# Kernel tuning notes

Measured on AMD Instinct MI355X. Metric: run time of the kernel, lower is better.

## Reference

```python
import jax, jax.numpy as jnp
import numpy as np

P = 16         # patch size
D = 192        # embed dim (vit_tiny)
NH = 3         # heads
DEPTH = 12
HID = 768      # mlp hidden = 4*D
NCLS = 1000
PCT = 0.25
EPS = 1e-6


def _ln(x, s, b):
    m = x.mean(-1, keepdims=True)
    v = ((x - m) ** 2).mean(-1, keepdims=True)
    return (x - m) * jax.lax.rsqrt(v + EPS) * s + b


def setup_inputs() -> dict:
    key = jax.random.key(0)
    ks = jax.random.split(key, 24)
    B, IMG = 64, 384
    std = 0.02
    d = {
        "magno_image": jax.random.normal(ks[0], (B, 3, IMG, IMG), jnp.float32),
        "line_drawing": jax.random.uniform(ks[1], (B, 1, IMG, IMG), jnp.float32),
        "conv_w": jax.random.normal(ks[2], (D, 3, P, P), jnp.float32) * std,
        "conv_b": jnp.zeros((D,), jnp.float32),
        "pos_embed": jax.random.normal(ks[3], (1, (IMG // P) ** 2 + 1, D), jnp.float32) * std,
        "cls_token": jax.random.normal(ks[4], (1, 1, D), jnp.float32) * std,
        "ln1_s": jnp.ones((DEPTH, D), jnp.float32),
        "ln1_b": jnp.zeros((DEPTH, D), jnp.float32),
        "qkv_w": jax.random.normal(ks[5], (DEPTH, D, 3 * D), jnp.float32) * std,
        "qkv_b": jnp.zeros((DEPTH, 3 * D), jnp.float32),
        "proj_w": jax.random.normal(ks[6], (DEPTH, D, D), jnp.float32) * std,
        "proj_b": jnp.zeros((DEPTH, D), jnp.float32),
        "ln2_s": jnp.ones((DEPTH, D), jnp.float32),
        "ln2_b": jnp.zeros((DEPTH, D), jnp.float32),
        "fc1_w": jax.random.normal(ks[7], (DEPTH, D, HID), jnp.float32) * std,
        "fc1_b": jnp.zeros((DEPTH, HID), jnp.float32),
        "fc2_w": jax.random.normal(ks[8], (DEPTH, HID, D), jnp.float32) * std,
        "fc2_b": jnp.zeros((DEPTH, D), jnp.float32),
        "normf_s": jnp.ones((D,), jnp.float32),
        "normf_b": jnp.zeros((D,), jnp.float32),
        "head_w": jax.random.normal(ks[9], (D, NCLS), jnp.float32) * std,
        "head_b": jnp.zeros((NCLS,), jnp.float32),
    }
    return d


def _forward(magno_image, line_drawing, conv_w, conv_b, pos_embed, cls_token,
             ln1_s, ln1_b, qkv_w, qkv_b, proj_w, proj_b, ln2_s, ln2_b,
             fc1_w, fc1_b, fc2_w, fc2_b, normf_s, normf_b, head_w, head_b):
    B, _, IMG, _ = magno_image.shape
    g = IMG // P
    N = g * g
    k = int(N * PCT)
    hd = D // NH

    # --- PatchImportanceScorer: avg-pool(patch_size) then flatten ---
    scores = line_drawing.reshape(B, g, P, g, P).mean(axis=(2, 4)).reshape(B, N)

    # --- patch embed (conv stride == kernel == reshaped matmul) ---
    x = magno_image.reshape(B, 3, g, P, g, P).transpose(0, 2, 4, 1, 3, 5)
    patches = x.reshape(B, N, 3 * P * P) @ conv_w.reshape(D, 3 * P * P).T + conv_b

    # --- top_k selection + gather of patches and pos-embed ---
    _, idx = jax.lax.top_k(scores, k)                      # (B, k)
    sel = jnp.take_along_axis(patches, idx[:, :, None], axis=1)
    pos = jnp.take_along_axis(
        jnp.broadcast_to(pos_embed[:, 1:, :], (B, N, D)), idx[:, :, None], axis=1)
    sel = sel + pos

    cls = jnp.broadcast_to(cls_token + pos_embed[:, :1, :], (B, 1, D))
    seq = jnp.concatenate([cls, sel], axis=1)              # (B, 1+k, D)
    S = 1 + k

    def block(h, p):
        l1s, l1b, qw, qb, pw, pb, l2s, l2b, f1w, f1b, f2w, f2b = p
        y = _ln(h, l1s, l1b)
        qkv = (y @ qw + qb).reshape(B, S, 3, NH, hd)
        q, kk, v = qkv[:, :, 0], qkv[:, :, 1], qkv[:, :, 2]  # (B,S,NH,hd)
        att = jnp.einsum('bqhd,bkhd->bhqk', q, kk) / np.sqrt(hd).astype(np.float32)
        att = jax.nn.softmax(att, axis=-1)
        o = jnp.einsum('bhqk,bkhd->bqhd', att, v).reshape(B, S, D)
        h = h + o @ pw + pb
        y = _ln(h, l2s, l2b)
        h = h + jax.nn.gelu(y @ f1w + f1b, approximate=False) @ f2w + f2b
        return h, None

    seq, _ = jax.lax.scan(block, seq, (ln1_s, ln1_b, qkv_w, qkv_b, proj_w, proj_b,
                                       ln2_s, ln2_b, fc1_w, fc1_b, fc2_w, fc2_b))
    seq = _ln(seq, normf_s, normf_b)
    return seq[:, 0] @ head_w + head_b


def reference(magno_image, line_drawing, conv_w, conv_b, pos_embed, cls_token,
              ln1_s, ln1_b, qkv_w, qkv_b, proj_w, proj_b, ln2_s, ln2_b,
              fc1_w, fc1_b, fc2_w, fc2_b, normf_s, normf_b, head_w, head_b):
    return _forward(magno_image, line_drawing, conv_w, conv_b, pos_embed, cls_token,
                    ln1_s, ln1_b, qkv_w, qkv_b, proj_w, proj_b, ln2_s, ln2_b,
                    fc1_w, fc1_b, fc2_w, fc2_b, normf_s, normf_b, head_w, head_b)
```

## Files before the change

kernel.cpp:

```cpp
#include <hip/hip_runtime.h>
#include <hip/hip_bf16.h>
#include <cmath>


#define Bsz   64
#define NPATCH 576
#define KSEL  144
#define SEQ   145
#define DIM   192
#define HIDN  768

typedef __bf16 bf16x8 __attribute__((ext_vector_type(8)));
typedef float  f32x4  __attribute__((ext_vector_type(4)));

__global__ __launch_bounds__(256) void scores_kernel(const float* __restrict__ line,
                                                     float* __restrict__ scores)
{
    int gp = blockIdx.x;
    int b = gp / NPATCH, p = gp % NPATCH;
    int gy = p / 24, gx = p % 24;
    int t = threadIdx.x, py = t >> 4, px = t & 15;
    float v = line[((size_t)b * 384 + gy * 16 + py) * 384 + gx * 16 + px];
    for (int off = 32; off; off >>= 1) v += __shfl_xor(v, off);
    __shared__ float red[4];
    if ((t & 63) == 0) red[t >> 6] = v;
    __syncthreads();
    if (t == 0) scores[gp] = (red[0] + red[1] + red[2] + red[3]) * (1.f / 256.f);
}

__global__ __launch_bounds__(256) void topk_kernel(const float* __restrict__ scores,
                                                   int* __restrict__ idx)
{
    int b = blockIdx.x;
    __shared__ float s[NPATCH];
    for (int i = threadIdx.x; i < NPATCH; i += 256) s[i] = scores[b * NPATCH + i];
    __syncthreads();
    for (int i = threadIdx.x; i < NPATCH; i += 256) {
        float si = s[i];
        int cnt = 0;
        for (int j = 0; j < NPATCH; ++j) {
            float sj = s[j];
            cnt += (sj > si) || (sj == si && j < i);
        }
        if (cnt < KSEL) idx[b * KSEL + cnt] = i;
    }
}

__global__ __launch_bounds__(256) void gather_kernel(const float* __restrict__ magno,
                                                     const int* __restrict__ idx,
                                                     __hip_bfloat16* __restrict__ selp)
{
    int bs = blockIdx.x;
    int b = bs / KSEL;
    int pi = idx[bs];
    int gy = pi / 24, gx = pi % 24;
    int t = threadIdx.x, py = t >> 4, px = t & 15;
    size_t src = ((size_t)b * 3 * 384 + gy * 16 + py) * 384 + gx * 16 + px;
    __hip_bfloat16* dst = &selp[(size_t)bs * 768];
#pragma unroll
    for (int c = 0; c < 3; ++c)
        dst[c * 256 + t] = __float2bfloat16(magno[src + (size_t)c * 384 * 384]);
}

__global__ __launch_bounds__(256) void convert_bf16_kernel(const float* __restrict__ src,
                                                           __hip_bfloat16* __restrict__ dst,
                                                           int n)
{
    int i = blockIdx.x * 256 + threadIdx.x;
    if (i < n) dst[i] = __float2bfloat16(src[i]);
}

__global__ __launch_bounds__(256) void transpose_w_kernel(const float* __restrict__ src,
                                                          __hip_bfloat16* __restrict__ dst,
                                                          int R, int C)
{
    __shared__ float t[32][33];
    size_t lo = (size_t)blockIdx.z * R * C;
    int r0 = blockIdx.y * 32, c0 = blockIdx.x * 32;
    int tx = threadIdx.x & 31, ty = threadIdx.x >> 5;
#pragma unroll
    for (int i = 0; i < 32; i += 8)
        t[ty + i][tx] = src[lo + (size_t)(r0 + ty + i) * C + c0 + tx];
    __syncthreads();
#pragma unroll
    for (int i = 0; i < 32; i += 8)
        dst[lo + (size_t)(c0 + ty + i) * R + r0 + tx] = __float2bfloat16(t[tx][ty + i]);
}

__global__ void cls_kernel(const float* __restrict__ cls, const float* __restrict__ pos,
                           float* __restrict__ h)
{
    int b = blockIdx.x, t = threadIdx.x;
    h[(size_t)b * SEQ * DIM + t] = cls[t] + pos[t];
}

__global__ __launch_bounds__(256) void ln_kernel(const float* __restrict__ x,
                                                 const float* __restrict__ s,
                                                 const float* __restrict__ bia,
                                                 __hip_bfloat16* __restrict__ y, int ntok)
{
    int w = threadIdx.x >> 6, lane = threadIdx.x & 63;
    int tok = blockIdx.x * 4 + w;
    if (tok >= ntok) return;
    const float* xp = &x[(size_t)tok * DIM];
    float x0 = xp[lane], x1 = xp[lane + 64], x2 = xp[lane + 128];
    float sum = x0 + x1 + x2;
    for (int off = 32; off; off >>= 1) sum += __shfl_xor(sum, off);
    float mean = sum * (1.f / 192.f);
    float d0 = x0 - mean, d1 = x1 - mean, d2 = x2 - mean;
    float vs = d0 * d0 + d1 * d1 + d2 * d2;
    for (int off = 32; off; off >>= 1) vs += __shfl_xor(vs, off);
    float rs = rsqrtf(vs * (1.f / 192.f) + 1e-6f);
    __hip_bfloat16* yp = &y[(size_t)tok * DIM];
    yp[lane]       = __float2bfloat16(d0 * rs * s[lane]       + bia[lane]);
    yp[lane + 64]  = __float2bfloat16(d1 * rs * s[lane + 64]  + bia[lane + 64]);
    yp[lane + 128] = __float2bfloat16(d2 * rs * s[lane + 128] + bia[lane + 128]);
}

template <int MODE>
__global__ __launch_bounds__(256) void gemm_bf16(const __hip_bfloat16* __restrict__ A,
                                                 const __hip_bfloat16* __restrict__ Wt,
                                                 const float* __restrict__ bias,
                                                 void* __restrict__ Cout,
                                                 int M, int N, int K,
                                                 const int* __restrict__ selidx,
                                                 const float* __restrict__ pos)
{
    __shared__ __align__(16) char As[8192];
    __shared__ __align__(16) char Bs[8192];
    const int tid = threadIdx.x;
    const int lane = tid & 63, wid = tid >> 6;
    const int wr = wid >> 1, wc = wid & 1;
    const int lr = lane & 15, lk = lane >> 4;
    const int m0 = blockIdx.y * 64, n0 = blockIdx.x * 64;
    f32x4 acc[2][2] = {};

    for (int k0 = 0; k0 < K; k0 += 64) {
#pragma unroll
        for (int it = 0; it < 2; ++it) {
            int chunk = it * 256 + tid;
            int r = chunk >> 3, g = chunk & 7;
            int loff = r * 128 + ((g ^ (r & 7)) * 16);
            *reinterpret_cast<uint4*>(As + loff) =
                *reinterpret_cast<const uint4*>(&A[(size_t)(m0 + r) * K + k0 + g * 8]);
            *reinterpret_cast<uint4*>(Bs + loff) =
                *reinterpret_cast<const uint4*>(&Wt[(size_t)(n0 + r) * K + k0 + g * 8]);
        }
        __syncthreads();
#pragma unroll
        for (int kc = 0; kc < 2; ++kc) {
            int g = kc * 4 + lk;
            bf16x8 af[2], bfr[2];
#pragma unroll
            for (int mi = 0; mi < 2; ++mi) {
                int r = wr * 32 + mi * 16 + lr;
                af[mi] = *reinterpret_cast<const bf16x8*>(As + r * 128 + ((g ^ (r & 7)) * 16));
            }
#pragma unroll
            for (int ni = 0; ni < 2; ++ni) {
                int r = wc * 32 + ni * 16 + lr;
                bfr[ni] = *reinterpret_cast<const bf16x8*>(Bs + r * 128 + ((g ^ (r & 7)) * 16));
            }
#pragma unroll
            for (int mi = 0; mi < 2; ++mi)
#pragma unroll
                for (int ni = 0; ni < 2; ++ni)
                    acc[mi][ni] = __builtin_amdgcn_mfma_f32_16x16x32_bf16(
                        af[mi], bfr[ni], acc[mi][ni], 0, 0, 0);
        }
        __syncthreads();
    }

#pragma unroll
    for (int mi = 0; mi < 2; ++mi)
#pragma unroll
    for (int ni = 0; ni < 2; ++ni)
#pragma unroll
    for (int j = 0; j < 4; ++j) {
        int row = m0 + wr * 32 + mi * 16 + (lane >> 4) * 4 + j;
        int col = n0 + wc * 32 + ni * 16 + (lane & 15);
        float v = acc[mi][ni][j] + bias[col];
        if (MODE == 0) {
            ((__hip_bfloat16*)Cout)[(size_t)row * N + col] = __float2bfloat16(v);
        } else if (MODE == 2) {
            ((__hip_bfloat16*)Cout)[(size_t)row * N + col] =
                __float2bfloat16(0.5f * v * (1.f + erff(v * 0.70710678118654752f)));
        } else {
            int bb2 = row / KSEL, ss = row % KSEL;
            int pi = selidx[row];
            v += pos[(size_t)(1 + pi) * DIM + col];
            ((float*)Cout)[((size_t)bb2 * SEQ + 1 + ss) * DIM + col] = v;
        }
    }
}

__global__ __launch_bounds__(256) void gemm_vt(const __hip_bfloat16* __restrict__ A,
                                               const __hip_bfloat16* __restrict__ Wt,
                                               const float* __restrict__ bias,
                                               __hip_bfloat16* __restrict__ Vt)
{
    __shared__ __align__(16) char As[8192];
    __shared__ __align__(16) char Bs[8192];
    const int tid = threadIdx.x;
    const int lane = tid & 63, wid = tid >> 6;
    const int wr = wid >> 1, wc = wid & 1;
    const int lr = lane & 15, lk = lane >> 4;
    const int m0 = blockIdx.y * 64, n0 = blockIdx.x * 64;
    const int K = DIM;
    f32x4 acc[2][2] = {};

    for (int k0 = 0; k0 < K; k0 += 64) {
#pragma unroll
        for (int it = 0; it < 2; ++it) {
            int chunk = it * 256 + tid;
            int r = chunk >> 3, g = chunk & 7;
            int loff = r * 128 + ((g ^ (r & 7)) * 16);
            *reinterpret_cast<uint4*>(As + loff) =
                *reinterpret_cast<const uint4*>(&A[(size_t)(m0 + r) * K + k0 + g * 8]);
            *reinterpret_cast<uint4*>(Bs + loff) =
                *reinterpret_cast<const uint4*>(&Wt[(size_t)(n0 + r) * K + k0 + g * 8]);
        }
        __syncthreads();
#pragma unroll
        for (int kc = 0; kc < 2; ++kc) {
            int g = kc * 4 + lk;
            bf16x8 af[2], bfr[2];
#pragma unroll
            for (int mi = 0; mi < 2; ++mi) {
                int r = wr * 32 + mi * 16 + lr;
                af[mi] = *reinterpret_cast<const bf16x8*>(As + r * 128 + ((g ^ (r & 7)) * 16));
            }
#pragma unroll
            for (int ni = 0; ni < 2; ++ni) {
                int r = wc * 32 + ni * 16 + lr;
                bfr[ni] = *reinterpret_cast<const bf16x8*>(Bs + r * 128 + ((g ^ (r & 7)) * 16));
            }
#pragma unroll
            for (int mi = 0; mi < 2; ++mi)
#pragma unroll
                for (int ni = 0; ni < 2; ++ni)
                    acc[mi][ni] = __builtin_amdgcn_mfma_f32_16x16x32_bf16(
                        af[mi], bfr[ni], acc[mi][ni], 0, 0, 0);
        }
        __syncthreads();
    }

#pragma unroll
    for (int mi = 0; mi < 2; ++mi)
#pragma unroll
    for (int ni = 0; ni < 2; ++ni)
#pragma unroll
    for (int j = 0; j < 4; ++j) {
        int row = m0 + wr * 32 + mi * 16 + (lane >> 4) * 4 + j;
        int c   = n0 + wc * 32 + ni * 16 + (lane & 15);
        float v = acc[mi][ni][j] + bias[c];
        int b = row / SEQ, s = row - b * SEQ;
        Vt[((size_t)(b * 3 + (c >> 6)) * 64 + (c & 63)) * 160 + s] = __float2bfloat16(v);
    }
}

template <bool DO_LN>
__global__ __launch_bounds__(256) void gemm_res_ln(const __hip_bfloat16* __restrict__ A,
                                                   const __hip_bfloat16* __restrict__ Wt,
                                                   const float* __restrict__ bias,
                                                   float* __restrict__ h,
                                                   const float* __restrict__ ls,
                                                   const float* __restrict__ lb,
                                                   __hip_bfloat16* __restrict__ y,
                                                   int K)
{
    __shared__ __align__(16) char As[8192];
    __shared__ __align__(16) char Bs[24576];
    const int tid = threadIdx.x;
    const int lane = tid & 63, w = tid >> 6;
    const int lr = lane & 15, lg = lane >> 4;
    const int m0 = blockIdx.x * 64;
    f32x4 acc[12] = {};

    for (int k0 = 0; k0 < K; k0 += 64) {
        {
            int chunk = tid;
#pragma unroll
            for (int it = 0; it < 2; ++it, chunk += 256) {
                int r = chunk >> 3, g = chunk & 7;
                *reinterpret_cast<uint4*>(As + r * 128 + ((g ^ (r & 7)) * 16)) =
                    *reinterpret_cast<const uint4*>(&A[(size_t)(m0 + r) * K + k0 + g * 8]);
            }
        }
        {
            int chunk = tid;
#pragma unroll
            for (int it = 0; it < 6; ++it, chunk += 256) {
                int r = chunk >> 3, g = chunk & 7;
                *reinterpret_cast<uint4*>(Bs + r * 128 + ((g ^ (r & 7)) * 16)) =
                    *reinterpret_cast<const uint4*>(&Wt[(size_t)r * K + k0 + g * 8]);
            }
        }
        __syncthreads();
#pragma unroll
        for (int kc = 0; kc < 2; ++kc) {
            int g = kc * 4 + lg;
            int ar = w * 16 + lr;
            bf16x8 af = *reinterpret_cast<const bf16x8*>(As + ar * 128 + ((g ^ (ar & 7)) * 16));
#pragma unroll
            for (int nf = 0; nf < 12; ++nf) {
                int br = nf * 16 + lr;
                bf16x8 bfv = *reinterpret_cast<const bf16x8*>(Bs + br * 128 + ((g ^ (br & 7)) * 16));
                acc[nf] = __builtin_amdgcn_mfma_f32_16x16x32_bf16(af, bfv, acc[nf], 0, 0, 0);
            }
        }
        __syncthreads();
    }

    float v[12][4];
    float sum[4] = {0.f, 0.f, 0.f, 0.f};
#pragma unroll
    for (int nf = 0; nf < 12; ++nf) {
        int col = nf * 16 + lr;
#pragma unroll
        for (int j = 0; j < 4; ++j) {
            int row = m0 + w * 16 + lg * 4 + j;
            float t = acc[nf][j] + bias[col] + h[(size_t)row * DIM + col];
            v[nf][j] = t;
            h[(size_t)row * DIM + col] = t;
            sum[j] += t;
        }
    }
    if (DO_LN) {
#pragma unroll
        for (int j = 0; j < 4; ++j)
            for (int off = 1; off < 16; off <<= 1) sum[j] += __shfl_xor(sum[j], off);
        float mean[4], sq[4] = {0.f, 0.f, 0.f, 0.f};
#pragma unroll
        for (int j = 0; j < 4; ++j) mean[j] = sum[j] * (1.f / 192.f);
#pragma unroll
        for (int nf = 0; nf < 12; ++nf)
#pragma unroll
            for (int j = 0; j < 4; ++j) {
                float d = v[nf][j] - mean[j];
                sq[j] += d * d;
            }
#pragma unroll
        for (int j = 0; j < 4; ++j) {
            for (int off = 1; off < 16; off <<= 1) sq[j] += __shfl_xor(sq[j], off);
            sq[j] = rsqrtf(sq[j] * (1.f / 192.f) + 1e-6f);
        }
#pragma unroll
        for (int nf = 0; nf < 12; ++nf) {
            int col = nf * 16 + lr;
            float sc = ls[col], bc = lb[col];
#pragma unroll
            for (int j = 0; j < 4; ++j) {
                int row = m0 + w * 16 + lg * 4 + j;
                y[(size_t)row * DIM + col] =
                    __float2bfloat16((v[nf][j] - mean[j]) * sq[j] * sc + bc);
            }
        }
    }
}

__global__ __launch_bounds__(128) void attn3_kernel(const __hip_bfloat16* __restrict__ qk,
                                                    const __hip_bfloat16* __restrict__ Vt,
                                                    __hip_bfloat16* __restrict__ o)
{
    const int b = blockIdx.y;
    const int h = blockIdx.x / 5, qt = blockIdx.x % 5;
    const int tid = threadIdx.x;
    const int wq = tid >> 6, lane = tid & 63;
    const int lr = lane & 15, lg = lane >> 4;
    __shared__ __hip_bfloat16 Ps[2][16][168];

    const size_t qbase = (size_t)b * SEQ * 384;
    const int q0 = qt * 32 + wq * 16;

    bf16x8 aq[2];
#pragma unroll
    for (int ks = 0; ks < 2; ++ks)
        aq[ks] = *reinterpret_cast<const bf16x8*>(
            &qk[qbase + (size_t)(q0 + lr) * 384 + h * 64 + ks * 32 + lg * 8]);

    f32x4 sc[10];
#pragma unroll
    for (int nf = 0; nf < 10; ++nf) sc[nf] = (f32x4){0.f, 0.f, 0.f, 0.f};
#pragma unroll
    for (int nf = 0; nf < 10; ++nf) {
        int key = nf * 16 + lr;
#pragma unroll
        for (int ks = 0; ks < 2; ++ks) {
            bf16x8 bk = *reinterpret_cast<const bf16x8*>(
                &qk[qbase + (size_t)key * 384 + 192 + h * 64 + ks * 32 + lg * 8]);
            sc[nf] = __builtin_amdgcn_mfma_f32_16x16x32_bf16(aq[ks], bk, sc[nf], 0, 0, 0);
        }
    }

    float mx[4] = {-1e30f, -1e30f, -1e30f, -1e30f};
#pragma unroll
    for (int nf = 0; nf < 10; ++nf) {
        bool valid = nf * 16 + lr < SEQ;
#pragma unroll
        for (int j = 0; j < 4; ++j) {
            float v = valid ? sc[nf][j] * 0.125f : -1e30f;
            sc[nf][j] = v;
            mx[j] = fmaxf(mx[j], v);
        }
    }
#pragma unroll
    for (int j = 0; j < 4; ++j)
        for (int off = 1; off < 16; off <<= 1)
            mx[j] = fmaxf(mx[j], __shfl_xor(mx[j], off));
    float sm[4] = {0.f, 0.f, 0.f, 0.f};
#pragma unroll
    for (int nf = 0; nf < 10; ++nf)
#pragma unroll
        for (int j = 0; j < 4; ++j) {
            float p = __expf(sc[nf][j] - mx[j]);
            sc[nf][j] = p;
            sm[j] += p;
        }
#pragma unroll
    for (int j = 0; j < 4; ++j) {
        for (int off = 1; off < 16; off <<= 1) sm[j] += __shfl_xor(sm[j], off);
        sm[j] = 1.f / sm[j];
    }
#pragma unroll
    for (int nf = 0; nf < 10; ++nf) {
        int key = nf * 16 + lr;
#pragma unroll
        for (int j = 0; j < 4; ++j)
            Ps[wq][lg * 4 + j][key] = __float2bfloat16(sc[nf][j] * sm[j]);
    }
    __syncthreads();

    const __hip_bfloat16* vtb = &Vt[(size_t)(b * 3 + h) * 64 * 160];
    f32x4 oacc[4];
#pragma unroll
    for (int nf = 0; nf < 4; ++nf) oacc[nf] = (f32x4){0.f, 0.f, 0.f, 0.f};
#pragma unroll
    for (int ks = 0; ks < 5; ++ks) {
        bf16x8 ap = *reinterpret_cast<const bf16x8*>(&Ps[wq][lr][ks * 32 + lg * 8]);
#pragma unroll
        for (int nf = 0; nf < 4; ++nf) {
            bf16x8 bv = *reinterpret_cast<const bf16x8*>(
                &vtb[(size_t)(nf * 16 + lr) * 160 + ks * 32 + lg * 8]);
            oacc[nf] = __builtin_amdgcn_mfma_f32_16x16x32_bf16(ap, bv, oacc[nf], 0, 0, 0);
        }
    }
#pragma unroll
    for (int nf = 0; nf < 4; ++nf)
#pragma unroll
        for (int j = 0; j < 4; ++j) {
            int q = q0 + lg * 4 + j;
            if (q < SEQ)
                o[((size_t)b * SEQ + q) * DIM + h * 64 + nf * 16 + lr] =
                    __float2bfloat16(oacc[nf][j]);
        }
}

__global__ __launch_bounds__(256) void head_kernel(const float* __restrict__ h,
                                                   const float* __restrict__ nfs,
                                                   const float* __restrict__ nfb,
                                                   const float* __restrict__ hw,
                                                   const float* __restrict__ hb,
                                                   float* __restrict__ out)
{
    int b = blockIdx.x, t = threadIdx.x;
    __shared__ float y[DIM];
    __shared__ float red[4];
    float x = (t < DIM) ? h[(size_t)b * SEQ * DIM + t] : 0.f;
    float sum = x;
    for (int off = 32; off; off >>= 1) sum += __shfl_xor(sum, off);
    if ((t & 63) == 0) red[t >> 6] = sum;
    __syncthreads();
    float mean = (red[0] + red[1] + red[2] + red[3]) * (1.f / 192.f);
    __syncthreads();
    float d = (t < DIM) ? (x - mean) : 0.f;
    float v = d * d;
    for (int off = 32; off; off >>= 1) v += __shfl_xor(v, off);
    if ((t & 63) == 0) red[t >> 6] = v;
    __syncthreads();
    float var = (red[0] + red[1] + red[2] + red[3]) * (1.f / 192.f);
    float rs = rsqrtf(var + 1e-6f);
    if (t < DIM) y[t] = d * rs * nfs[t] + nfb[t];
    __syncthreads();
    for (int n = t; n < 1000; n += 256) {
        float acc = hb[n];
#pragma unroll 8
        for (int k = 0; k < DIM; ++k)
            acc = fmaf(y[k], hw[(size_t)k * 1000 + n], acc);
        out[(size_t)b * 1000 + n] = acc;
    }
}

extern "C" void kernel_launch(void* const* d_in, const int* in_sizes, int n_in,
                              void* d_out, int out_size, void* d_ws, size_t ws_size,
                              hipStream_t stream)
{
    const float* magno  = (const float*)d_in[0];
    const float* line   = (const float*)d_in[1];
    const float* conv_w = (const float*)d_in[2];
    const float* conv_b = (const float*)d_in[3];
    const float* pos    = (const float*)d_in[4];
    const float* cls    = (const float*)d_in[5];
    const float* ln1_s  = (const float*)d_in[6];
    const float* ln1_b  = (const float*)d_in[7];
    const float* qkv_w  = (const float*)d_in[8];
    const float* qkv_b  = (const float*)d_in[9];
    const float* proj_w = (const float*)d_in[10];
    const float* proj_b = (const float*)d_in[11];
    const float* ln2_s  = (const float*)d_in[12];
    const float* ln2_b  = (const float*)d_in[13];
    const float* fc1_w  = (const float*)d_in[14];
    const float* fc1_b  = (const float*)d_in[15];
    const float* fc2_w  = (const float*)d_in[16];
    const float* fc2_b  = (const float*)d_in[17];
    const float* normf_s = (const float*)d_in[18];
    const float* normf_b = (const float*)d_in[19];
    const float* head_w = (const float*)d_in[20];
    const float* head_b = (const float*)d_in[21];
    float* out = (float*)d_out;
    (void)in_sizes; (void)n_in; (void)out_size; (void)ws_size;

    char* ws = (char*)d_ws;
    int*            idx     = (int*)            (ws + 0);
    float*          h       = (float*)          (ws + 147456);
    __hip_bfloat16* y       = (__hip_bfloat16*) (ws + 7274496);
    __hip_bfloat16* qk      = (__hip_bfloat16*) (ws + 10838016);
    __hip_bfloat16* Vt      = (__hip_bfloat16*) (ws + 17965056);
    __hip_bfloat16* tbuf    = (__hip_bfloat16*) (ws + 21897216);
    __hip_bfloat16* wt_qkv  = (__hip_bfloat16*) (ws + 36151296);
    __hip_bfloat16* wt_proj = (__hip_bfloat16*) (ws + 38805504);
    __hip_bfloat16* wt_fc1  = (__hip_bfloat16*) (ws + 39690240);
    __hip_bfloat16* wt_fc2  = (__hip_bfloat16*) (ws + 43229184);
    float*          scoresbuf = (float*)qk;
    __hip_bfloat16* convT     = y;
    __hip_bfloat16* selp      = tbuf;

    hipMemsetAsync(Vt, 0, 3932160, stream);
    transpose_w_kernel<<<dim3(18, 6, 12), 256, 0, stream>>>(qkv_w, wt_qkv, DIM, 576);
    transpose_w_kernel<<<dim3(6, 6, 12),  256, 0, stream>>>(proj_w, wt_proj, DIM, DIM);
    transpose_w_kernel<<<dim3(24, 6, 12), 256, 0, stream>>>(fc1_w, wt_fc1, DIM, HIDN);
    transpose_w_kernel<<<dim3(6, 24, 12), 256, 0, stream>>>(fc2_w, wt_fc2, HIDN, DIM);
    convert_bf16_kernel<<<576, 256, 0, stream>>>(conv_w, convT, DIM * 768);

    scores_kernel<<<Bsz * NPATCH, 256, 0, stream>>>(line, scoresbuf);
    topk_kernel<<<Bsz, 256, 0, stream>>>(scoresbuf, idx);
    gather_kernel<<<Bsz * KSEL, 256, 0, stream>>>(magno, idx, selp);
    cls_kernel<<<Bsz, DIM, 0, stream>>>(cls, pos, h);
    gemm_bf16<3><<<dim3(3, 144), 256, 0, stream>>>(selp, convT, conv_b, h,
                                                   9216, DIM, 768, idx, pos);

    const int ntok = Bsz * SEQ;
    ln_kernel<<<ntok / 4, 256, 0, stream>>>(h, ln1_s, ln1_b, y, ntok);
    for (int l = 0; l < 12; ++l) {
        gemm_bf16<0><<<dim3(6, 145), 256, 0, stream>>>(y, wt_qkv + (size_t)l * 576 * DIM,
                                                       qkv_b + l * 576, qk,
                                                       ntok, 384, DIM, nullptr, nullptr);
        gemm_vt<<<dim3(3, 145), 256, 0, stream>>>(y, wt_qkv + (size_t)l * 576 * DIM + 384 * DIM,
                                                  qkv_b + l * 576 + 384, Vt);
        attn3_kernel<<<dim3(15, Bsz), 128, 0, stream>>>(qk, Vt, y);
        gemm_res_ln<true><<<145, 256, 0, stream>>>(y, wt_proj + (size_t)l * DIM * DIM,
                                                   proj_b + l * DIM, h,
                                                   ln2_s + l * DIM, ln2_b + l * DIM, y, DIM);
        gemm_bf16<2><<<dim3(12, 145), 256, 0, stream>>>(y, wt_fc1 + (size_t)l * HIDN * DIM,
                                                        fc1_b + l * HIDN, tbuf,
                                                        ntok, HIDN, DIM, nullptr, nullptr);
        if (l < 11)
            gemm_res_ln<true><<<145, 256, 0, stream>>>(tbuf, wt_fc2 + (size_t)l * DIM * HIDN,
                                                       fc2_b + l * DIM, h,
                                                       ln1_s + (l + 1) * DIM, ln1_b + (l + 1) * DIM,
                                                       y, HIDN);
        else
            gemm_res_ln<false><<<145, 256, 0, stream>>>(tbuf, wt_fc2 + (size_t)l * DIM * HIDN,
                                                        fc2_b + l * DIM, h,
                                                        nullptr, nullptr, y, HIDN);
    }
    head_kernel<<<Bsz, 256, 0, stream>>>(h, normf_s, normf_b, head_w, head_b, out);
}
```

Baseline: 969.9 us.

## Fuse QKV GEMMs into one launch and fuse attention with projection+residual+LayerNorm

Merges the separate QK and V GEMM launches into a single gemm_qkv kernel that routes output columns to either the qk buffer or the transposed V buffer. Replaces the attention kernel plus the proj/residual/LN GEMM with one attnproj kernel: three waves compute per-head attention for 32 queries into shared memory, then all four waves do the output projection, add the residual and compute LayerNorm in-block. This removes two launches per layer and the round-trip of the attention output through global memory. In exchange, the attention grid drops from 960 to 320 blocks, the fourth wave idles during attention, and projection weights are re-read from global per block without LDS staging.

Result: faster. 940.8 us (-3.0%).

```diff
diff --git a/kernel.cpp b/kernel.cpp
--- a/kernel.cpp
+++ b/kernel.cpp
@@ -180,9 +180,7 @@
         int row = m0 + wr * 32 + mi * 16 + (lane >> 4) * 4 + j;
         int col = n0 + wc * 32 + ni * 16 + (lane & 15);
         float v = acc[mi][ni][j] + bias[col];
-        if (MODE == 0) {
-            ((__hip_bfloat16*)Cout)[(size_t)row * N + col] = __float2bfloat16(v);
-        } else if (MODE == 2) {
+        if (MODE == 2) {
             ((__hip_bfloat16*)Cout)[(size_t)row * N + col] =
                 __float2bfloat16(0.5f * v * (1.f + erff(v * 0.70710678118654752f)));
         } else {
@@ -194,10 +192,11 @@
     }
 }
 
-__global__ __launch_bounds__(256) void gemm_vt(const __hip_bfloat16* __restrict__ A,
-                                               const __hip_bfloat16* __restrict__ Wt,
-                                               const float* __restrict__ bias,
-                                               __hip_bfloat16* __restrict__ Vt)
+__global__ __launch_bounds__(256) void gemm_qkv(const __hip_bfloat16* __restrict__ A,
+                                                const __hip_bfloat16* __restrict__ Wt,
+                                                const float* __restrict__ bias,
+                                                __hip_bfloat16* __restrict__ qk,
+                                                __hip_bfloat16* __restrict__ Vt)
 {
     __shared__ __align__(16) char As[8192];
     __shared__ __align__(16) char Bs[8192];
@@ -252,10 +251,208 @@
 #pragma unroll
     for (int j = 0; j < 4; ++j) {
         int row = m0 + wr * 32 + mi * 16 + (lane >> 4) * 4 + j;
-        int c   = n0 + wc * 32 + ni * 16 + (lane & 15);
-        float v = acc[mi][ni][j] + bias[c];
-        int b = row / SEQ, s = row - b * SEQ;
-        Vt[((size_t)(b * 3 + (c >> 6)) * 64 + (c & 63)) * 160 + s] = __float2bfloat16(v);
+        int col = n0 + wc * 32 + ni * 16 + (lane & 15);
+        float v = acc[mi][ni][j] + bias[col];
+        if (col < 384) {
+            qk[(size_t)row * 384 + col] = __float2bfloat16(v);
+        } else {
+            int c = col - 384;
+            int b = row / SEQ, s = row - b * SEQ;
+            Vt[((size_t)(b * 3 + (c >> 6)) * 64 + (c & 63)) * 160 + s] = __float2bfloat16(v);
+        }
+    }
+}
+
+__global__ __launch_bounds__(256) void attnproj_kernel(const __hip_bfloat16* __restrict__ qk,
+                                                       const __hip_bfloat16* __restrict__ Vt,
+                                                       const __hip_bfloat16* __restrict__ Wp,
+                                                       const float* __restrict__ pbias,
+                                                       float* __restrict__ h,
+                                                       const float* __restrict__ ls,
+                                                       const float* __restrict__ lb,
+                                                       __hip_bfloat16* __restrict__ y)
+{
+    const int b = blockIdx.y, qt = blockIdx.x;
+    const int tid = threadIdx.x;
+    const int w = tid >> 6, lane = tid & 63;
+    const int lr = lane & 15, lg = lane >> 4;
+    __shared__ __hip_bfloat16 Ps[3][32][168];
+    __shared__ __hip_bfloat16 Ot[32][200];
+    __shared__ float redsum[4][32];
+    __shared__ float redsq[4][32];
+
+    const size_t qbase = (size_t)b * SEQ * 384;
+    const int q0 = qt * 32;
+
+    if (w < 3) {
+        const int hh = w;
+        bf16x8 aq[2][2];
+#pragma unroll
+        for (int mi = 0; mi < 2; ++mi)
+#pragma unroll
+            for (int ks = 0; ks < 2; ++ks)
+                aq[mi][ks] = *reinterpret_cast<const bf16x8*>(
+                    &qk[qbase + (size_t)(q0 + mi * 16 + lr) * 384 + hh * 64 + ks * 32 + lg * 8]);
+        f32x4 sc[2][10];
+#pragma unroll
+        for (int mi = 0; mi < 2; ++mi)
+#pragma unroll
+            for (int nf = 0; nf < 10; ++nf) sc[mi][nf] = (f32x4){0.f, 0.f, 0.f, 0.f};
+#pragma unroll
+        for (int nf = 0; nf < 10; ++nf) {
+            int key = nf * 16 + lr;
+#pragma unroll
+            for (int ks = 0; ks < 2; ++ks) {
+                bf16x8 bk = *reinterpret_cast<const bf16x8*>(
+                    &qk[qbase + (size_t)key * 384 + 192 + hh * 64 + ks * 32 + lg * 8]);
+#pragma unroll
+                for (int mi = 0; mi < 2; ++mi)
+                    sc[mi][nf] = __builtin_amdgcn_mfma_f32_16x16x32_bf16(
+                        aq[mi][ks], bk, sc[mi][nf], 0, 0, 0);
+            }
+        }
+#pragma unroll
+        for (int mi = 0; mi < 2; ++mi) {
+            float mx[4] = {-1e30f, -1e30f, -1e30f, -1e30f};
+#pragma unroll
+            for (int nf = 0; nf < 10; ++nf) {
+                bool valid = nf * 16 + lr < SEQ;
+#pragma unroll
+                for (int j = 0; j < 4; ++j) {
+                    float v = valid ? sc[mi][nf][j] * 0.125f : -1e30f;
+                    sc[mi][nf][j] = v;
+                    mx[j] = fmaxf(mx[j], v);
+                }
+            }
+#pragma unroll
+            for (int j = 0; j < 4; ++j)
+                for (int off = 1; off < 16; off <<= 1)
+                    mx[j] = fmaxf(mx[j], __shfl_xor(mx[j], off));
+            float sm[4] = {0.f, 0.f, 0.f, 0.f};
+#pragma unroll
+            for (int nf = 0; nf < 10; ++nf)
+#pragma unroll
+                for (int j = 0; j < 4; ++j) {
+                    float p = __expf(sc[mi][nf][j] - mx[j]);
+                    sc[mi][nf][j] = p;
+                    sm[j] += p;
+                }
+#pragma unroll
+            for (int j = 0; j < 4; ++j) {
+                for (int off = 1; off < 16; off <<= 1) sm[j] += __shfl_xor(sm[j], off);
+                sm[j] = 1.f / sm[j];
+            }
+#pragma unroll
+            for (int nf = 0; nf < 10; ++nf) {
+                int key = nf * 16 + lr;
+#pragma unroll
+                for (int j = 0; j < 4; ++j)
+                    Ps[hh][mi * 16 + lg * 4 + j][key] = __float2bfloat16(sc[mi][nf][j] * sm[j]);
+            }
+        }
+        const __hip_bfloat16* vtb = &Vt[(size_t)(b * 3 + hh) * 64 * 160];
+        f32x4 oacc[2][4];
+#pragma unroll
+        for (int mi = 0; mi < 2; ++mi)
+#pragma unroll
+            for (int nf = 0; nf < 4; ++nf) oacc[mi][nf] = (f32x4){0.f, 0.f, 0.f, 0.f};
+#pragma unroll
+        for (int ks = 0; ks < 5; ++ks) {
+            bf16x8 ap[2];
+            ap[0] = *reinterpret_cast<const bf16x8*>(&Ps[hh][lr][ks * 32 + lg * 8]);
+            ap[1] = *reinterpret_cast<const bf16x8*>(&Ps[hh][16 + lr][ks * 32 + lg * 8]);
+#pragma unroll
+            for (int nf = 0; nf < 4; ++nf) {
+                bf16x8 bv = *reinterpret_cast<const bf16x8*>(
+                    &vtb[(size_t)(nf * 16 + lr) * 160 + ks * 32 + lg * 8]);
+#pragma unroll
+                for (int mi = 0; mi < 2; ++mi)
+                    oacc[mi][nf] = __builtin_amdgcn_mfma_f32_16x16x32_bf16(
+                        ap[mi], bv, oacc[mi][nf], 0, 0, 0);
+            }
+        }
+#pragma unroll
+        for (int mi = 0; mi < 2; ++mi)
+#pragma unroll
+            for (int nf = 0; nf < 4; ++nf)
+#pragma unroll
+                for (int j = 0; j < 4; ++j)
+                    Ot[mi * 16 + lg * 4 + j][hh * 64 + nf * 16 + lr] =
+                        __float2bfloat16(oacc[mi][nf][j]);
+    }
+    __syncthreads();
+
+    f32x4 pacc[2][3];
+#pragma unroll
+    for (int mi = 0; mi < 2; ++mi)
+#pragma unroll
+        for (int nf = 0; nf < 3; ++nf) pacc[mi][nf] = (f32x4){0.f, 0.f, 0.f, 0.f};
+#pragma unroll
+    for (int kk = 0; kk < 6; ++kk) {
+        bf16x8 af[2];
+        af[0] = *reinterpret_cast<const bf16x8*>(&Ot[lr][kk * 32 + lg * 8]);
+        af[1] = *reinterpret_cast<const bf16x8*>(&Ot[16 + lr][kk * 32 + lg * 8]);
+#pragma unroll
+        for (int nf = 0; nf < 3; ++nf) {
+            int ncol = w * 48 + nf * 16 + lr;
+            bf16x8 bw = *reinterpret_cast<const bf16x8*>(&Wp[(size_t)ncol * 192 + kk * 32 + lg * 8]);
+#pragma unroll
+            for (int mi = 0; mi < 2; ++mi)
+                pacc[mi][nf] = __builtin_amdgcn_mfma_f32_16x16x32_bf16(
+                    af[mi], bw, pacc[mi][nf], 0, 0, 0);
+        }
+    }
+    float v[2][3][4];
+    float psum[2][4] = {}, psq[2][4] = {};
+#pragma unroll
+    for (int mi = 0; mi < 2; ++mi)
+#pragma unroll
+    for (int nf = 0; nf < 3; ++nf) {
+        int col = w * 48 + nf * 16 + lr;
+        float bcol = pbias[col];
+#pragma unroll
+        for (int j = 0; j < 4; ++j) {
+            int q = q0 + mi * 16 + lg * 4 + j;
+            float res = (q < SEQ) ? h[((size_t)b * SEQ + q) * DIM + col] : 0.f;
+            float t = pacc[mi][nf][j] + bcol + res;
+            v[mi][nf][j] = t;
+            psum[mi][j] += t;
+            psq[mi][j] += t * t;
+        }
+    }
+#pragma unroll
+    for (int mi = 0; mi < 2; ++mi)
+#pragma unroll
+        for (int j = 0; j < 4; ++j) {
+            for (int off = 1; off < 16; off <<= 1) {
+                psum[mi][j] += __shfl_xor(psum[mi][j], off);
+                psq[mi][j]  += __shfl_xor(psq[mi][j], off);
+            }
+            redsum[w][mi * 16 + lg * 4 + j] = psum[mi][j];
+            redsq[w][mi * 16 + lg * 4 + j]  = psq[mi][j];
+        }
+    __syncthreads();
+#pragma unroll
+    for (int mi = 0; mi < 2; ++mi) {
+#pragma unroll
+        for (int j = 0; j < 4; ++j) {
+            int r = mi * 16 + lg * 4 + j;
+            int q = q0 + r;
+            if (q >= SEQ) continue;
+            float tsum = redsum[0][r] + redsum[1][r] + redsum[2][r] + redsum[3][r];
+            float tsq  = redsq[0][r]  + redsq[1][r]  + redsq[2][r]  + redsq[3][r];
+            float mean = tsum * (1.f / 192.f);
+            float var  = tsq * (1.f / 192.f) - mean * mean;
+            float rs = rsqrtf(var + 1e-6f);
+#pragma unroll
+            for (int nf = 0; nf < 3; ++nf) {
+                int col = w * 48 + nf * 16 + lr;
+                float t = v[mi][nf][j];
+                h[((size_t)b * SEQ + q) * DIM + col] = t;
+                y[((size_t)b * SEQ + q) * DIM + col] =
+                    __float2bfloat16((t - mean) * rs * ls[col] + lb[col]);
+            }
+        }
     }
 }
 
@@ -357,103 +554,6 @@
             }
         }
     }
-}
-
-__global__ __launch_bounds__(128) void attn3_kernel(const __hip_bfloat16* __restrict__ qk,
-                                                    const __hip_bfloat16* __restrict__ Vt,
-                                                    __hip_bfloat16* __restrict__ o)
-{
-    const int b = blockIdx.y;
-    const int h = blockIdx.x / 5, qt = blockIdx.x % 5;
-    const int tid = threadIdx.x;
-    const int wq = tid >> 6, lane = tid & 63;
-    const int lr = lane & 15, lg = lane >> 4;
-    __shared__ __hip_bfloat16 Ps[2][16][168];
-
-    const size_t qbase = (size_t)b * SEQ * 384;
-    const int q0 = qt * 32 + wq * 16;
-
-    bf16x8 aq[2];
-#pragma unroll
-    for (int ks = 0; ks < 2; ++ks)
-        aq[ks] = *reinterpret_cast<const bf16x8*>(
-            &qk[qbase + (size_t)(q0 + lr) * 384 + h * 64 + ks * 32 + lg * 8]);
-
-    f32x4 sc[10];
-#pragma unroll
-    for (int nf = 0; nf < 10; ++nf) sc[nf] = (f32x4){0.f, 0.f, 0.f, 0.f};
-#pragma unroll
-    for (int nf = 0; nf < 10; ++nf) {
-        int key = nf * 16 + lr;
-#pragma unroll
-        for (int ks = 0; ks < 2; ++ks) {
-            bf16x8 bk = *reinterpret_cast<const bf16x8*>(
-                &qk[qbase + (size_t)key * 384 + 192 + h * 64 + ks * 32 + lg * 8]);
-            sc[nf] = __builtin_amdgcn_mfma_f32_16x16x32_bf16(aq[ks], bk, sc[nf], 0, 0, 0);
-        }
-    }
-
-    float mx[4] = {-1e30f, -1e30f, -1e30f, -1e30f};
-#pragma unroll
-    for (int nf = 0; nf < 10; ++nf) {
-        bool valid = nf * 16 + lr < SEQ;
-#pragma unroll
-        for (int j = 0; j < 4; ++j) {
-            float v = valid ? sc[nf][j] * 0.125f : -1e30f;
-            sc[nf][j] = v;
-            mx[j] = fmaxf(mx[j], v);
-        }
-    }
-#pragma unroll
-    for (int j = 0; j < 4; ++j)
-        for (int off = 1; off < 16; off <<= 1)
-            mx[j] = fmaxf(mx[j], __shfl_xor(mx[j], off));
-    float sm[4] = {0.f, 0.f, 0.f, 0.f};
-#pragma unroll
-    for (int nf = 0; nf < 10; ++nf)
-#pragma unroll
-        for (int j = 0; j < 4; ++j) {
-            float p = __expf(sc[nf][j] - mx[j]);
-            sc[nf][j] = p;
-            sm[j] += p;
-        }
-#pragma unroll
-    for (int j = 0; j < 4; ++j) {
-        for (int off = 1; off < 16; off <<= 1) sm[j] += __shfl_xor(sm[j], off);
-        sm[j] = 1.f / sm[j];
-    }
-#pragma unroll
-    for (int nf = 0; nf < 10; ++nf) {
-        int key = nf * 16 + lr;
-#pragma unroll
-        for (int j = 0; j < 4; ++j)
-            Ps[wq][lg * 4 + j][key] = __float2bfloat16(sc[nf][j] * sm[j]);
-    }
-    __syncthreads();
-
-    const __hip_bfloat16* vtb = &Vt[(size_t)(b * 3 + h) * 64 * 160];
-    f32x4 oacc[4];
-#pragma unroll
-    for (int nf = 0; nf < 4; ++nf) oacc[nf] = (f32x4){0.f, 0.f, 0.f, 0.f};
-#pragma unroll
-    for (int ks = 0; ks < 5; ++ks) {
-        bf16x8 ap = *reinterpret_cast<const bf16x8*>(&Ps[wq][lr][ks * 32 + lg * 8]);
-#pragma unroll
-        for (int nf = 0; nf < 4; ++nf) {
-            bf16x8 bv = *reinterpret_cast<const bf16x8*>(
-                &vtb[(size_t)(nf * 16 + lr) * 160 + ks * 32 + lg * 8]);
-            oacc[nf] = __builtin_amdgcn_mfma_f32_16x16x32_bf16(ap, bv, oacc[nf], 0, 0, 0);
-        }
-    }
-#pragma unroll
-    for (int nf = 0; nf < 4; ++nf)
-#pragma unroll
-        for (int j = 0; j < 4; ++j) {
-            int q = q0 + lg * 4 + j;
-            if (q < SEQ)
-                o[((size_t)b * SEQ + q) * DIM + h * 64 + nf * 16 + lr] =
-                    __float2bfloat16(oacc[nf][j]);
-        }
 }
 
 __global__ __launch_bounds__(256) void head_kernel(const float* __restrict__ h,
@@ -552,15 +652,12 @@
     const int ntok = Bsz * SEQ;
     ln_kernel<<<ntok / 4, 256, 0, stream>>>(h, ln1_s, ln1_b, y, ntok);
     for (int l = 0; l < 12; ++l) {
-        gemm_bf16<0><<<dim3(6, 145), 256, 0, stream>>>(y, wt_qkv + (size_t)l * 576 * DIM,
-                                                       qkv_b + l * 576, qk,
-                                                       ntok, 384, DIM, nullptr, nullptr);
-        gemm_vt<<<dim3(3, 145), 256, 0, stream>>>(y, wt_qkv + (size_t)l * 576 * DIM + 384 * DIM,
-                                                  qkv_b + l * 576 + 384, Vt);
-        attn3_kernel<<<dim3(15, Bsz), 128, 0, stream>>>(qk, Vt, y);
-        gemm_res_ln<true><<<145, 256, 0, stream>>>(y, wt_proj + (size_t)l * DIM * DIM,
-                                                   proj_b + l * DIM, h,
-                                                   ln2_s + l * DIM, ln2_b + l * DIM, y, DIM);
+        gemm_qkv<<<dim3(9, 145), 256, 0, stream>>>(y, wt_qkv + (size_t)l * 576 * DIM,
+                                                   qkv_b + l * 576, qk, Vt);
+        attnproj_kernel<<<dim3(5, Bsz), 256, 0, stream>>>(qk, Vt,
+                                                          wt_proj + (size_t)l * DIM * DIM,
+                                                          proj_b + l * DIM, h,
+                                                          ln2_s + l * DIM, ln2_b + l * DIM, y);
         gemm_bf16<2><<<dim3(12, 145), 256, 0, stream>>>(y, wt_fc1 + (size_t)l * HIDN * DIM,
                                                         fc1_b + l * HIDN, tbuf,
                                                         ntok, HIDN, DIM, nullptr, nullptr);
```
